# Performance work log

Measured on AMD Instinct MI355X. Metric: run time of the kernel, lower is better.

The kernel has to match this reference:

```python
import jax, jax.numpy as jnp
import numpy as np

N = 100_000       # nodes
E = 1_600_000     # edges (avg degree 16)
D = 64            # in_dim
H = 64            # hidden width (hidden_channels = [64,64,64,64] -> 3 GCN layers)
L = 3             # num GCNConv layers
END = 128         # end_channels
EPS = 1e-5        # batchnorm eps


def setup_inputs() -> dict:
    key = jax.random.key(0)
    ks = jax.random.split(key, 8)

    def lin(k, fi, fo):
        return (jax.random.normal(k, (fi, fo), jnp.float32) / np.sqrt(fi)).astype(jnp.float32)

    X = jax.random.normal(ks[0], (N, D), jnp.float32)
    edge_index = jax.random.randint(ks[1], (2, E), 0, N)
    W_in = lin(ks[2], D, H)
    b_in = jnp.zeros((H,), jnp.float32)
    Ws = (jax.random.normal(ks[3], (L, H, H), jnp.float32) / np.sqrt(H)).astype(jnp.float32)
    bs = jnp.zeros((L, H), jnp.float32)
    gammas = jnp.ones((L, H), jnp.float32)
    betas = jnp.zeros((L, H), jnp.float32)
    W1 = lin(ks[4], H, END)
    b1 = jnp.zeros((END,), jnp.float32)
    W2 = lin(ks[5], END, 1)
    b2 = jnp.zeros((1,), jnp.float32)
    return dict(X=X, edge_index=edge_index, W_in=W_in, b_in=b_in, Ws=Ws, bs=bs,
                gammas=gammas, betas=betas, W1=W1, b1=b1, W2=W2, b2=b2)


def reference(X, edge_index, W_in, b_in, Ws, bs, gammas, betas, W1, b1, W2, b2):
    src, dst = edge_index[0], edge_index[1]
    # symmetric GCN normalization with self-loops: deg includes the self-loop (+1)
    deg = jax.ops.segment_sum(jnp.ones((E,), X.dtype), dst, num_segments=N) + 1.0
    dinv = jax.lax.rsqrt(deg)                      # deg^{-1/2}
    norm = dinv[src] * dinv[dst]                   # [E]
    self_norm = (dinv * dinv)[:, None]             # deg^{-1} for self-loop edges, [N,1]

    x = X @ W_in + b_in                            # input Linear
    for i in range(L):
        h = x @ Ws[i]                              # [N, H]
        # gather -> weight -> scatter-add (neighbor aggregation) + self-loop term + bias
        agg = jax.ops.segment_sum(h[src] * norm[:, None], dst, num_segments=N)
        h = agg + h * self_norm + bs[i]
        # BatchNorm over nodes (training-mode batch statistics)
        mean = jnp.mean(h, axis=0)
        var = jnp.var(h, axis=0)
        h = gammas[i] * (h - mean) * jax.lax.rsqrt(var + EPS) + betas[i]
        if i < L - 1:
            h = jax.nn.relu(h)
        x = h
    # OutputLayer: Linear -> act -> Linear(n_steps=1), binary=False -> no sigmoid
    h = jax.nn.relu(x @ W1 + b1)
    return h @ W2 + b2
```

## Files before the change

kernel.cpp:

```cpp
#include <hip/hip_runtime.h>

#define NN 100000
#define NE 1600000
#define NB_SCAN 391

__device__ inline float b2f(unsigned short u) {
  return __uint_as_float(((unsigned)u) << 16);
}
__device__ inline unsigned short f2b(float f) {
  unsigned x = __float_as_uint(f);
  unsigned r = (x + 0x7fffu + ((x >> 16) & 1u)) >> 16;
  return (unsigned short)r;
}


__global__ void count_rank_kernel(const int* __restrict__ dst, int* __restrict__ counts,
                                  int* __restrict__ rank) {
  int i = blockIdx.x * blockDim.x + threadIdx.x;
  int st = gridDim.x * blockDim.x;
  for (; i < NE; i += st) rank[i] = atomicAdd(&counts[dst[i]], 1);
}

__global__ void scan1_kernel(const int* __restrict__ counts, int* __restrict__ offsets,
                             int* __restrict__ blocksum, float* __restrict__ dinv) {
  __shared__ int s[256];
  int t = threadIdx.x;
  int i = blockIdx.x * 256 + t;
  int v = (i < NN) ? counts[i] : 0;
  s[t] = v; __syncthreads();
  for (int off = 1; off < 256; off <<= 1) {
    int x = 0;
    if (t >= off) x = s[t - off];
    __syncthreads();
    if (t >= off) s[t] += x;
    __syncthreads();
  }
  if (i < NN) {
    offsets[i] = s[t] - v;
    dinv[i] = rsqrtf((float)v + 1.0f);
  }
  if (t == 255) blocksum[blockIdx.x] = s[255];
}

__global__ void scan2_kernel(const int* __restrict__ blocksum, int* __restrict__ blockpfx,
                             int* __restrict__ offsets) {
  __shared__ int s[512];
  int t = threadIdx.x;
  int v = (t < NB_SCAN) ? blocksum[t] : 0;
  s[t] = v; __syncthreads();
  for (int off = 1; off < 512; off <<= 1) {
    int x = 0;
    if (t >= off) x = s[t - off];
    __syncthreads();
    if (t >= off) s[t] += x;
    __syncthreads();
  }
  if (t < NB_SCAN) blockpfx[t] = s[t] - v;
  if (t == 511) offsets[NN] = s[511];
}

__global__ void scan3_kernel(int* __restrict__ offsets, const int* __restrict__ blockpfx) {
  int i = blockIdx.x * 256 + threadIdx.x;
  if (i < NN) offsets[i] += blockpfx[i >> 8];
}

__global__ void scatter_kernel(const int* __restrict__ src, const int* __restrict__ dst,
                               const int* __restrict__ offsets, const int* __restrict__ rank,
                               int* __restrict__ src_s) {
  int i = blockIdx.x * blockDim.x + threadIdx.x;
  int st = gridDim.x * blockDim.x;
  for (; i < NE; i += st) {
    int d = dst[i];
    src_s[offsets[d] + rank[i]] = src[i];
  }
}

__global__ void foldw_kernel(const float* __restrict__ W_in, const float* __restrict__ b_in,
                             const float* __restrict__ W0,
                             float* __restrict__ Wc, float* __restrict__ bc) {
  int t = threadIdx.x;
  for (int e = t; e < 4096; e += 256) {
    int i = e >> 6, j = e & 63;
    float s = 0.f;
#pragma unroll
    for (int k = 0; k < 64; ++k) s += W_in[i * 64 + k] * W0[k * 64 + j];
    Wc[e] = s;
  }
  if (t < 64) {
    float s = 0.f;
#pragma unroll
    for (int k = 0; k < 64; ++k) s += b_in[k] * W0[k * 64 + t];
    bc[t] = s;
  }
}


__global__ __launch_bounds__(256) void gemm64_kernel(
    const void* __restrict__ xin, int xbf16,
    const float* __restrict__ W, const float* __restrict__ bias,
    const float* __restrict__ bnac, const float* __restrict__ rowscale,
    unsigned short* __restrict__ out16) {
  __shared__ float sW[64][64];
  __shared__ float sx[16][64];
  int t = threadIdx.x;
  int col = t & 63;
  int rw = t >> 6;
  int row0 = blockIdx.x * 16;

#pragma unroll
  for (int j = 0; j < 16; ++j) {
    int e = t + 256 * j;
    sW[e >> 6][col] = W[e];
  }
  float a = 1.f, c = 0.f;
  if (bnac) { a = bnac[col]; c = bnac[64 + col]; }
  const float* xf = (const float*)xin;
  const unsigned short* xh = (const unsigned short*)xin;
#pragma unroll
  for (int j = 0; j < 4; ++j) {
    int e = t + 256 * j;
    int r = e >> 6;
    int grow = row0 + r;
    float v = 0.f;
    if (grow < NN)
      v = xbf16 ? b2f(xh[(size_t)grow * 64 + col]) : xf[(size_t)grow * 64 + col];
    if (bnac) v = fmaxf(fmaf(v, a, c), 0.f);
    sx[r][col] = v;
  }
  __syncthreads();

  float acc0 = 0, acc1 = 0, acc2 = 0, acc3 = 0;
#pragma unroll 4
  for (int k = 0; k < 64; k += 4) {
    float4 x0 = *(const float4*)&sx[rw * 4 + 0][k];
    float4 x1 = *(const float4*)&sx[rw * 4 + 1][k];
    float4 x2 = *(const float4*)&sx[rw * 4 + 2][k];
    float4 x3 = *(const float4*)&sx[rw * 4 + 3][k];
    float w0 = sW[k + 0][col], w1 = sW[k + 1][col];
    float w2 = sW[k + 2][col], w3 = sW[k + 3][col];
    acc0 = fmaf(x0.w, w3, fmaf(x0.z, w2, fmaf(x0.y, w1, fmaf(x0.x, w0, acc0))));
    acc1 = fmaf(x1.w, w3, fmaf(x1.z, w2, fmaf(x1.y, w1, fmaf(x1.x, w0, acc1))));
    acc2 = fmaf(x2.w, w3, fmaf(x2.z, w2, fmaf(x2.y, w1, fmaf(x2.x, w0, acc2))));
    acc3 = fmaf(x3.w, w3, fmaf(x3.z, w2, fmaf(x3.y, w1, fmaf(x3.x, w0, acc3))));
  }
  float bv = bias ? bias[col] : 0.f;
  int r0 = row0 + rw * 4;
#pragma unroll
  for (int r = 0; r < 4; ++r) {
    int grow = r0 + r;
    if (grow < NN) {
      float acc = (r == 0) ? acc0 : (r == 1) ? acc1 : (r == 2) ? acc2 : acc3;
      out16[(size_t)grow * 64 + col] = f2b((acc + bv) * rowscale[grow]);
    }
  }
}


__device__ __forceinline__ void agg_slow(const unsigned short* __restrict__ xp16,
                                         const int* __restrict__ src_s,
                                         int beg, int end, int lane,
                                         float& a0, float& a1, float& a2, float& a3) {
  int deg = end - beg, done = 0;
  while (done < deg) {
    int chunk = deg - done;
    if (chunk > 64) chunk = 64;
    int idx = (lane < chunk) ? src_s[beg + done + lane] : 0;
    int j = 0;
    for (; j + 4 <= chunk; j += 4) {
      int t0 = __shfl(idx, j + 0), t1 = __shfl(idx, j + 1);
      int t2 = __shfl(idx, j + 2), t3 = __shfl(idx, j + 3);
      a0 += b2f(xp16[(size_t)t0 * 64 + lane]);
      a1 += b2f(xp16[(size_t)t1 * 64 + lane]);
      a2 += b2f(xp16[(size_t)t2 * 64 + lane]);
      a3 += b2f(xp16[(size_t)t3 * 64 + lane]);
    }
    for (; j < chunk; ++j) {
      int s = __shfl(idx, j);
      a0 += b2f(xp16[(size_t)s * 64 + lane]);
    }
    done += chunk;
  }
}

__global__ __launch_bounds__(256) void agg_kernel(
    const unsigned short* __restrict__ xp16, const int* __restrict__ offsets,
    const int* __restrict__ src_s, const float* __restrict__ dinv,
    const float* __restrict__ bvec, unsigned short* __restrict__ h2,
    float* __restrict__ bnacc) {
  int t = threadIdx.x;
  int lane = t & 63;
  int wv = t >> 6;
  float bias = bvec[lane];
  float s1 = 0.f, s2 = 0.f;
  int gw = blockIdx.x * 4 + wv;
  int nw = gridDim.x * 4;
  const int NP = NN / 2;
  for (int p = gw; p < NP; p += nw) {
    int nA = 2 * p, nB = 2 * p + 1;
    int begA = offsets[nA];
    int begB = offsets[nA + 1];
    int endB = offsets[nA + 2];
    int degA = begB - begA, degB = endB - begB;
    float a0 = b2f(xp16[(size_t)nA * 64 + lane]), a1 = 0.f, a2 = 0.f, a3 = 0.f;
    float c0 = b2f(xp16[(size_t)nB * 64 + lane]), c1 = 0.f, c2 = 0.f, c3 = 0.f;
    if (degA <= 64 && degB <= 64) {
      int idxA = (lane < degA) ? src_s[begA + lane] : 0;
      int idxB = (lane < degB) ? src_s[begB + lane] : 0;
      int ja = 0, jb = 0;
      while (ja + 8 <= degA && jb + 8 <= degB) {
        int A0 = __shfl(idxA, ja + 0), A1 = __shfl(idxA, ja + 1);
        int A2 = __shfl(idxA, ja + 2), A3 = __shfl(idxA, ja + 3);
        int A4 = __shfl(idxA, ja + 4), A5 = __shfl(idxA, ja + 5);
        int A6 = __shfl(idxA, ja + 6), A7 = __shfl(idxA, ja + 7);
        int B0 = __shfl(idxB, jb + 0), B1 = __shfl(idxB, jb + 1);
        int B2 = __shfl(idxB, jb + 2), B3 = __shfl(idxB, jb + 3);
        int B4 = __shfl(idxB, jb + 4), B5 = __shfl(idxB, jb + 5);
        int B6 = __shfl(idxB, jb + 6), B7 = __shfl(idxB, jb + 7);
        unsigned short uA0 = xp16[(size_t)A0 * 64 + lane];
        unsigned short uA1 = xp16[(size_t)A1 * 64 + lane];
        unsigned short uA2 = xp16[(size_t)A2 * 64 + lane];
        unsigned short uA3 = xp16[(size_t)A3 * 64 + lane];
        unsigned short uA4 = xp16[(size_t)A4 * 64 + lane];
        unsigned short uA5 = xp16[(size_t)A5 * 64 + lane];
        unsigned short uA6 = xp16[(size_t)A6 * 64 + lane];
        unsigned short uA7 = xp16[(size_t)A7 * 64 + lane];
        unsigned short uB0 = xp16[(size_t)B0 * 64 + lane];
        unsigned short uB1 = xp16[(size_t)B1 * 64 + lane];
        unsigned short uB2 = xp16[(size_t)B2 * 64 + lane];
        unsigned short uB3 = xp16[(size_t)B3 * 64 + lane];
        unsigned short uB4 = xp16[(size_t)B4 * 64 + lane];
        unsigned short uB5 = xp16[(size_t)B5 * 64 + lane];
        unsigned short uB6 = xp16[(size_t)B6 * 64 + lane];
        unsigned short uB7 = xp16[(size_t)B7 * 64 + lane];
        a0 += b2f(uA0) + b2f(uA4);  a1 += b2f(uA1) + b2f(uA5);
        a2 += b2f(uA2) + b2f(uA6);  a3 += b2f(uA3) + b2f(uA7);
        c0 += b2f(uB0) + b2f(uB4);  c1 += b2f(uB1) + b2f(uB5);
        c2 += b2f(uB2) + b2f(uB6);  c3 += b2f(uB3) + b2f(uB7);
        ja += 8; jb += 8;
      }
      for (; ja + 8 <= degA; ja += 8) {
        int A0 = __shfl(idxA, ja + 0), A1 = __shfl(idxA, ja + 1);
        int A2 = __shfl(idxA, ja + 2), A3 = __shfl(idxA, ja + 3);
        int A4 = __shfl(idxA, ja + 4), A5 = __shfl(idxA, ja + 5);
        int A6 = __shfl(idxA, ja + 6), A7 = __shfl(idxA, ja + 7);
        unsigned short u0 = xp16[(size_t)A0 * 64 + lane];
        unsigned short u1 = xp16[(size_t)A1 * 64 + lane];
        unsigned short u2 = xp16[(size_t)A2 * 64 + lane];
        unsigned short u3 = xp16[(size_t)A3 * 64 + lane];
        unsigned short u4 = xp16[(size_t)A4 * 64 + lane];
        unsigned short u5 = xp16[(size_t)A5 * 64 + lane];
        unsigned short u6 = xp16[(size_t)A6 * 64 + lane];
        unsigned short u7 = xp16[(size_t)A7 * 64 + lane];
        a0 += b2f(u0) + b2f(u4);  a1 += b2f(u1) + b2f(u5);
        a2 += b2f(u2) + b2f(u6);  a3 += b2f(u3) + b2f(u7);
      }
      for (; ja + 4 <= degA; ja += 4) {
        int A0 = __shfl(idxA, ja + 0), A1 = __shfl(idxA, ja + 1);
        int A2 = __shfl(idxA, ja + 2), A3 = __shfl(idxA, ja + 3);
        a0 += b2f(xp16[(size_t)A0 * 64 + lane]);
        a1 += b2f(xp16[(size_t)A1 * 64 + lane]);
        a2 += b2f(xp16[(size_t)A2 * 64 + lane]);
        a3 += b2f(xp16[(size_t)A3 * 64 + lane]);
      }
      for (; ja < degA; ++ja) {
        int s = __shfl(idxA, ja);
        a0 += b2f(xp16[(size_t)s * 64 + lane]);
      }
      for (; jb + 8 <= degB; jb += 8) {
        int B0 = __shfl(idxB, jb + 0), B1 = __shfl(idxB, jb + 1);
        int B2 = __shfl(idxB, jb + 2), B3 = __shfl(idxB, jb + 3);
        int B4 = __shfl(idxB, jb + 4), B5 = __shfl(idxB, jb + 5);
        int B6 = __shfl(idxB, jb + 6), B7 = __shfl(idxB, jb + 7);
        unsigned short u0 = xp16[(size_t)B0 * 64 + lane];
        unsigned short u1 = xp16[(size_t)B1 * 64 + lane];
        unsigned short u2 = xp16[(size_t)B2 * 64 + lane];
        unsigned short u3 = xp16[(size_t)B3 * 64 + lane];
        unsigned short u4 = xp16[(size_t)B4 * 64 + lane];
        unsigned short u5 = xp16[(size_t)B5 * 64 + lane];
        unsigned short u6 = xp16[(size_t)B6 * 64 + lane];
        unsigned short u7 = xp16[(size_t)B7 * 64 + lane];
        c0 += b2f(u0) + b2f(u4);  c1 += b2f(u1) + b2f(u5);
        c2 += b2f(u2) + b2f(u6);  c3 += b2f(u3) + b2f(u7);
      }
      for (; jb + 4 <= degB; jb += 4) {
        int B0 = __shfl(idxB, jb + 0), B1 = __shfl(idxB, jb + 1);
        int B2 = __shfl(idxB, jb + 2), B3 = __shfl(idxB, jb + 3);
        c0 += b2f(xp16[(size_t)B0 * 64 + lane]);
        c1 += b2f(xp16[(size_t)B1 * 64 + lane]);
        c2 += b2f(xp16[(size_t)B2 * 64 + lane]);
        c3 += b2f(xp16[(size_t)B3 * 64 + lane]);
      }
      for (; jb < degB; ++jb) {
        int s = __shfl(idxB, jb);
        c0 += b2f(xp16[(size_t)s * 64 + lane]);
      }
    } else {
      agg_slow(xp16, src_s, begA, begB, lane, a0, a1, a2, a3);
      agg_slow(xp16, src_s, begB, endB, lane, c0, c1, c2, c3);
    }
    float vA = ((a0 + a1) + (a2 + a3)) * dinv[nA] + bias;
    float vB = ((c0 + c1) + (c2 + c3)) * dinv[nB] + bias;
    h2[(size_t)nA * 64 + lane] = f2b(vA);
    h2[(size_t)nB * 64 + lane] = f2b(vB);
    s1 += vA + vB;
    s2 += vA * vA + vB * vB;
  }
  __shared__ float ls[4][2][64];
  ls[wv][0][lane] = s1;
  ls[wv][1][lane] = s2;
  __syncthreads();
  if (wv == 0) {
    float a = ls[0][0][lane] + ls[1][0][lane] + ls[2][0][lane] + ls[3][0][lane];
    float b = ls[0][1][lane] + ls[1][1][lane] + ls[2][1][lane] + ls[3][1][lane];
    atomicAdd(&bnacc[lane], a);
    atomicAdd(&bnacc[64 + lane], b);
  }
}

__global__ void bn_finalize_kernel(const float* __restrict__ bnacc,
                                   const float* __restrict__ gamma,
                                   const float* __restrict__ beta,
                                   float* __restrict__ bnac) {
  int ch = threadIdx.x;
  float mean = bnacc[ch] * (1.0f / NN);
  float var = bnacc[64 + ch] * (1.0f / NN) - mean * mean;
  float istd = rsqrtf(var + 1e-5f);
  float a = gamma[ch] * istd;
  bnac[ch] = a;
  bnac[64 + ch] = beta[ch] - mean * a;
}


__global__ __launch_bounds__(256) void out_kernel(
    const unsigned short* __restrict__ x, const float* __restrict__ bnac,
    const float* __restrict__ W1, const float* __restrict__ b1,
    const float* __restrict__ W2, const float* __restrict__ b2,
    float* __restrict__ out) {
  __shared__ float sW1[64][128];
  __shared__ float sx[16][64];
  __shared__ float sz[16][128];
  __shared__ float sW2[128];
  int t = threadIdx.x;
  int row0 = blockIdx.x * 16;
#pragma unroll
  for (int j = 0; j < 32; ++j) {
    int e = t + 256 * j;
    sW1[e >> 7][e & 127] = W1[e];
  }
  if (t < 128) sW2[t] = W2[t];
  {
    int c64 = t & 63;
    float a = bnac[c64], c = bnac[64 + c64];
#pragma unroll
    for (int j = 0; j < 4; ++j) {
      int e = t + 256 * j;
      int r = e >> 6;
      int grow = row0 + r;
      float v = (grow < NN) ? b2f(x[(size_t)grow * 64 + c64]) : 0.f;
      sx[r][c64] = fmaf(v, a, c);
    }
  }
  __syncthreads();

  int col = t & 127;
  int rg = t >> 7;
  float b1v = b1[col];
  float acc[8];
#pragma unroll
  for (int r = 0; r < 8; ++r) acc[r] = 0.f;
#pragma unroll 4
  for (int k = 0; k < 64; k += 4) {
    float w0 = sW1[k + 0][col], w1 = sW1[k + 1][col];
    float w2 = sW1[k + 2][col], w3 = sW1[k + 3][col];
#pragma unroll
    for (int r = 0; r < 8; ++r) {
      float4 xv = *(const float4*)&sx[rg * 8 + r][k];
      acc[r] = fmaf(xv.w, w3, fmaf(xv.z, w2, fmaf(xv.y, w1, fmaf(xv.x, w0, acc[r]))));
    }
  }
#pragma unroll
  for (int r = 0; r < 8; ++r) sz[rg * 8 + r][col] = fmaxf(acc[r] + b1v, 0.f);
  __syncthreads();

  {
    int row = t >> 4, g = t & 15;
    const float4* zr = (const float4*)&sz[row][0];
    const float4* wp = (const float4*)sW2;
    float4 z0 = zr[g * 2], z1 = zr[g * 2 + 1];
    float4 w0 = wp[g * 2], w1 = wp[g * 2 + 1];
    float p = z0.x * w0.x + z0.y * w0.y + z0.z * w0.z + z0.w * w0.w
            + z1.x * w1.x + z1.y * w1.y + z1.z * w1.z + z1.w * w1.w;
    p += __shfl_down(p, 8);
    p += __shfl_down(p, 4);
    p += __shfl_down(p, 2);
    p += __shfl_down(p, 1);
    int grow = row0 + row;
    if (g == 0 && grow < NN) out[grow] = p + b2[0];
  }
}


extern "C" void kernel_launch(void* const* d_in, const int* in_sizes, int n_in,
                              void* d_out, int out_size, void* d_ws, size_t ws_size,
                              hipStream_t stream) {
  const float* X = (const float*)d_in[0];
  const int* edge = (const int*)d_in[1];
  const int* esrc = edge;
  const int* edst = edge + NE;
  const float* W_in = (const float*)d_in[2];
  const float* b_in = (const float*)d_in[3];
  const float* Ws = (const float*)d_in[4];
  const float* bs = (const float*)d_in[5];
  const float* gammas = (const float*)d_in[6];
  const float* betas = (const float*)d_in[7];
  const float* W1 = (const float*)d_in[8];
  const float* b1 = (const float*)d_in[9];
  const float* W2 = (const float*)d_in[10];
  const float* b2 = (const float*)d_in[11];
  float* out = (float*)d_out;

  char* base = (char*)d_ws;
  size_t o = 0;
  auto alloc = [&](size_t bytes) {
    o = (o + 255) & ~(size_t)255;
    void* p = base + o;
    o += bytes;
    return p;
  };
  int* counts = (int*)alloc((size_t)NN * 4);
  int* offsets = (int*)alloc((size_t)(NN + 1) * 4);
  int* blocksum = (int*)alloc(512 * 4);
  int* blockpfx = (int*)alloc(512 * 4);
  int* rank = (int*)alloc((size_t)NE * 4);
  int* src_s = (int*)alloc((size_t)NE * 4);
  float* dinv = (float*)alloc((size_t)NN * 4);
  unsigned short* bufA = (unsigned short*)alloc((size_t)NN * 64 * 2);
  unsigned short* bufB = (unsigned short*)alloc((size_t)NN * 64 * 2);
  unsigned short* hbuf16 = (unsigned short*)alloc((size_t)NN * 64 * 2);
  float* bnacc = (float*)alloc(3 * 128 * 4);
  float* bnpar = (float*)alloc(3 * 128 * 4);
  float* Wc = (float*)alloc(4096 * 4);
  float* bc = (float*)alloc(64 * 4);

  hipMemsetAsync(counts, 0, (size_t)NN * 4, stream);
  hipMemsetAsync(bnacc, 0, 3 * 128 * 4, stream);

  foldw_kernel<<<1, 256, 0, stream>>>(W_in, b_in, Ws, Wc, bc);
  count_rank_kernel<<<2048, 256, 0, stream>>>(edst, counts, rank);
  scan1_kernel<<<NB_SCAN, 256, 0, stream>>>(counts, offsets, blocksum, dinv);
  scan2_kernel<<<1, 512, 0, stream>>>(blocksum, blockpfx, offsets);
  scan3_kernel<<<NB_SCAN, 256, 0, stream>>>(offsets, blockpfx);
  scatter_kernel<<<2048, 256, 0, stream>>>(esrc, edst, offsets, rank, src_s);

  const int GEMM_GRID = (NN + 15) / 16;
  unsigned short* xbufs[2] = {bufA, bufB};
  const unsigned short* xcur = nullptr;
  for (int i = 0; i < 3; ++i) {
    if (i == 0) {
      gemm64_kernel<<<GEMM_GRID, 256, 0, stream>>>(X, 0, Wc, bc, nullptr, dinv, hbuf16);
    } else {
      gemm64_kernel<<<GEMM_GRID, 256, 0, stream>>>(xcur, 1, Ws + (size_t)i * 64 * 64, nullptr,
                                                   bnpar + (size_t)(i - 1) * 128,
                                                   dinv, hbuf16);
    }
    unsigned short* xnext = xbufs[i & 1];
    agg_kernel<<<2048, 256, 0, stream>>>(hbuf16, offsets, src_s, dinv,
                                         bs + (size_t)i * 64, xnext,
                                         bnacc + (size_t)i * 128);
    bn_finalize_kernel<<<1, 64, 0, stream>>>(bnacc + (size_t)i * 128,
                                             gammas + (size_t)i * 64,
                                             betas + (size_t)i * 64,
                                             bnpar + (size_t)i * 128);
    xcur = xnext;
  }
  out_kernel<<<GEMM_GRID, 256, 0, stream>>>(xcur, bnpar + 2 * 128, W1, b1, W2, b2, out);
}
```

Baseline: 630.2 us.

## Replace scalar FP32 node GEMM with bf16 MFMA tiles, pre-convert X to bf16

The per-layer 64x64 node transform now uses a 16x16x32 bf16 MFMA kernel with weights held in registers, and each wave handles 16-row tiles in a grid-stride loop. The input features are first converted to bf16 by a separate kernel so that all three GEMMs read bf16. The aim is to cut the FP32 FMA cost and the shared-memory traffic of the old kernel. In exchange it adds an extra pass over X, and the first-layer input and the weights are rounded to bf16, which lowers precision.

```diff
diff --git a/kernel.cpp b/kernel.cpp
--- a/kernel.cpp
+++ b/kernel.cpp
@@ -3,6 +3,9 @@
 #define NN 100000
 #define NE 1600000
 #define NB_SCAN 391
+
+typedef __attribute__((ext_vector_type(8))) short bf16x8;
+typedef __attribute__((ext_vector_type(4))) float f32x4;
 
 __device__ inline float b2f(unsigned short u) {
   return __uint_as_float(((unsigned)u) << 16);
@@ -94,63 +97,91 @@
   }
 }
 
-
-__global__ __launch_bounds__(256) void gemm64_kernel(
-    const void* __restrict__ xin, int xbf16,
+__global__ __launch_bounds__(256) void cvtx_kernel(const float4* __restrict__ X4,
+                                                   ushort4* __restrict__ X16) {
+  int i = blockIdx.x * blockDim.x + threadIdx.x;
+  int st = gridDim.x * blockDim.x;
+  for (; i < NN * 16; i += st) {
+    float4 v = X4[i];
+    ushort4 o;
+    o.x = f2b(v.x); o.y = f2b(v.y); o.z = f2b(v.z); o.w = f2b(v.w);
+    X16[i] = o;
+  }
+}
+
+
+__global__ __launch_bounds__(256) void gemm_mfma_kernel(
+    const unsigned short* __restrict__ x16,
     const float* __restrict__ W, const float* __restrict__ bias,
-    const float* __restrict__ bnac, const float* __restrict__ rowscale,
+    const float* __restrict__ bnac, const float* __restrict__ dinv,
     unsigned short* __restrict__ out16) {
-  __shared__ float sW[64][64];
-  __shared__ float sx[16][64];
+  __shared__ float sW[4096];
   int t = threadIdx.x;
-  int col = t & 63;
-  int rw = t >> 6;
-  int row0 = blockIdx.x * 16;
-
-#pragma unroll
-  for (int j = 0; j < 16; ++j) {
-    int e = t + 256 * j;
-    sW[e >> 6][col] = W[e];
-  }
-  float a = 1.f, c = 0.f;
-  if (bnac) { a = bnac[col]; c = bnac[64 + col]; }
-  const float* xf = (const float*)xin;
-  const unsigned short* xh = (const unsigned short*)xin;
-#pragma unroll
-  for (int j = 0; j < 4; ++j) {
-    int e = t + 256 * j;
-    int r = e >> 6;
-    int grow = row0 + r;
-    float v = 0.f;
-    if (grow < NN)
-      v = xbf16 ? b2f(xh[(size_t)grow * 64 + col]) : xf[(size_t)grow * 64 + col];
-    if (bnac) v = fmaxf(fmaf(v, a, c), 0.f);
-    sx[r][col] = v;
-  }
+  int lane = t & 63;
+  int wv = t >> 6;
+#pragma unroll
+  for (int j = 0; j < 16; ++j) sW[t + 256 * j] = W[t + 256 * j];
   __syncthreads();
-
-  float acc0 = 0, acc1 = 0, acc2 = 0, acc3 = 0;
-#pragma unroll 4
-  for (int k = 0; k < 64; k += 4) {
-    float4 x0 = *(const float4*)&sx[rw * 4 + 0][k];
-    float4 x1 = *(const float4*)&sx[rw * 4 + 1][k];
-    float4 x2 = *(const float4*)&sx[rw * 4 + 2][k];
-    float4 x3 = *(const float4*)&sx[rw * 4 + 3][k];
-    float w0 = sW[k + 0][col], w1 = sW[k + 1][col];
-    float w2 = sW[k + 2][col], w3 = sW[k + 3][col];
-    acc0 = fmaf(x0.w, w3, fmaf(x0.z, w2, fmaf(x0.y, w1, fmaf(x0.x, w0, acc0))));
-    acc1 = fmaf(x1.w, w3, fmaf(x1.z, w2, fmaf(x1.y, w1, fmaf(x1.x, w0, acc1))));
-    acc2 = fmaf(x2.w, w3, fmaf(x2.z, w2, fmaf(x2.y, w1, fmaf(x2.x, w0, acc2))));
-    acc3 = fmaf(x3.w, w3, fmaf(x3.z, w2, fmaf(x3.y, w1, fmaf(x3.x, w0, acc3))));
-  }
-  float bv = bias ? bias[col] : 0.f;
-  int r0 = row0 + rw * 4;
-#pragma unroll
-  for (int r = 0; r < 4; ++r) {
-    int grow = r0 + r;
-    if (grow < NN) {
-      float acc = (r == 0) ? acc0 : (r == 1) ? acc1 : (r == 2) ? acc2 : acc3;
-      out16[(size_t)grow * 64 + col] = f2b((acc + bv) * rowscale[grow]);
+  int r16 = lane & 15;
+  int g4 = lane >> 4;
+
+  bf16x8 bf[4][2];
+#pragma unroll
+  for (int ct = 0; ct < 4; ++ct) {
+#pragma unroll
+    for (int kh = 0; kh < 2; ++kh) {
+#pragma unroll
+      for (int j = 0; j < 8; ++j) {
+        int k = kh * 32 + g4 * 8 + j;
+        bf[ct][kh][j] = (short)f2b(sW[k * 64 + ct * 16 + r16]);
+      }
+    }
+  }
+  float an[16], cn[16];
+  if (bnac) {
+#pragma unroll
+    for (int kh = 0; kh < 2; ++kh) {
+#pragma unroll
+      for (int j = 0; j < 8; ++j) {
+        int k = kh * 32 + g4 * 8 + j;
+        an[kh * 8 + j] = bnac[k];
+        cn[kh * 8 + j] = bnac[64 + k];
+      }
+    }
+  }
+  float bv[4];
+#pragma unroll
+  for (int ct = 0; ct < 4; ++ct) bv[ct] = bias ? bias[ct * 16 + r16] : 0.f;
+
+  const int NT = NN / 16;
+  int nw = gridDim.x * 4;
+  for (int tile = blockIdx.x * 4 + wv; tile < NT; tile += nw) {
+    int row0 = tile * 16;
+    const unsigned short* xr = x16 + (size_t)(row0 + r16) * 64 + g4 * 8;
+    bf16x8 alo = *(const bf16x8*)xr;
+    bf16x8 ahi = *(const bf16x8*)(xr + 32);
+    if (bnac) {
+#pragma unroll
+      for (int j = 0; j < 8; ++j) {
+        float v = fmaxf(fmaf(b2f((unsigned short)alo[j]), an[j], cn[j]), 0.f);
+        alo[j] = (short)f2b(v);
+        float w = fmaxf(fmaf(b2f((unsigned short)ahi[j]), an[8 + j], cn[8 + j]), 0.f);
+        ahi[j] = (short)f2b(w);
+      }
+    }
+    float dv[4];
+#pragma unroll
+    for (int r = 0; r < 4; ++r) dv[r] = dinv[row0 + g4 * 4 + r];
+#pragma unroll
+    for (int ct = 0; ct < 4; ++ct) {
+      f32x4 acc = {0.f, 0.f, 0.f, 0.f};
+      acc = __builtin_amdgcn_mfma_f32_16x16x32_bf16(alo, bf[ct][0], acc, 0, 0, 0);
+      acc = __builtin_amdgcn_mfma_f32_16x16x32_bf16(ahi, bf[ct][1], acc, 0, 0, 0);
+#pragma unroll
+      for (int r = 0; r < 4; ++r) {
+        int grow = row0 + g4 * 4 + r;
+        out16[(size_t)grow * 64 + ct * 16 + r16] = f2b((acc[r] + bv[ct]) * dv[r]);
+      }
     }
   }
 }
@@ -434,6 +465,7 @@
   int* rank = (int*)alloc((size_t)NE * 4);
   int* src_s = (int*)alloc((size_t)NE * 4);
   float* dinv = (float*)alloc((size_t)NN * 4);
+  unsigned short* X16 = (unsigned short*)alloc((size_t)NN * 64 * 2);
   unsigned short* bufA = (unsigned short*)alloc((size_t)NN * 64 * 2);
   unsigned short* bufB = (unsigned short*)alloc((size_t)NN * 64 * 2);
   unsigned short* hbuf16 = (unsigned short*)alloc((size_t)NN * 64 * 2);
@@ -446,6 +478,7 @@
   hipMemsetAsync(bnacc, 0, 3 * 128 * 4, stream);
 
   foldw_kernel<<<1, 256, 0, stream>>>(W_in, b_in, Ws, Wc, bc);
+  cvtx_kernel<<<2048, 256, 0, stream>>>((const float4*)X, (ushort4*)X16);
   count_rank_kernel<<<2048, 256, 0, stream>>>(edst, counts, rank);
   scan1_kernel<<<NB_SCAN, 256, 0, stream>>>(counts, offsets, blocksum, dinv);
   scan2_kernel<<<1, 512, 0, stream>>>(blocksum, blockpfx, offsets);
@@ -457,11 +490,11 @@
   const unsigned short* xcur = nullptr;
   for (int i = 0; i < 3; ++i) {
     if (i == 0) {
-      gemm64_kernel<<<GEMM_GRID, 256, 0, stream>>>(X, 0, Wc, bc, nullptr, dinv, hbuf16);
+      gemm_mfma_kernel<<<1563, 256, 0, stream>>>(X16, Wc, bc, nullptr, dinv, hbuf16);
     } else {
-      gemm64_kernel<<<GEMM_GRID, 256, 0, stream>>>(xcur, 1, Ws + (size_t)i * 64 * 64, nullptr,
-                                                   bnpar + (size_t)(i - 1) * 128,
-                                                   dinv, hbuf16);
+      gemm_mfma_kernel<<<1563, 256, 0, stream>>>(xcur, Ws + (size_t)i * 64 * 64, nullptr,
+                                                 bnpar + (size_t)(i - 1) * 128,
+                                                 dinv, hbuf16);
     }
     unsigned short* xnext = xbufs[i & 1];
     agg_kernel<<<2048, 256, 0, stream>>>(hbuf16, offsets, src_s, dinv,
```

New measurement: 589.7 us. 6.4% less time.
